# Kernel optimization log

Measured on AMD Instinct MI355X. Metric: run time of the kernel, lower is better.

The kernel has to match this reference:

```python
import jax, jax.numpy as jnp
import numpy as np

B, S, E, H = 2, 2048, 1024, 16
DH = E // H  # 64


def setup_inputs() -> dict:
    key = jax.random.key(0)
    ks = jax.random.split(key, 13)
    s = 1.0 / np.sqrt(E)
    inp = {
        'query': jax.random.normal(ks[0], (B, S, E), jnp.float32),
        'key':   jax.random.normal(ks[1], (B, S, E), jnp.float32),
        'value': jax.random.normal(ks[2], (B, S, E), jnp.float32),
        # nn.Linear weights stored [out, in]
        'Wq': jax.random.uniform(ks[3], (E, E), jnp.float32, -s, s),
        'bq': jax.random.uniform(ks[4], (E,), jnp.float32, -s, s),
        'Wk': jax.random.uniform(ks[5], (E, E), jnp.float32, -s, s),
        'bk': jax.random.uniform(ks[6], (E,), jnp.float32, -s, s),
        'Wv': jax.random.uniform(ks[7], (E, E), jnp.float32, -s, s),
        'bv': jax.random.uniform(ks[8], (E,), jnp.float32, -s, s),
        # 1x1 Conv2d over head channels: weight [H, H] (squeezed from [H,H,1,1]), bias [H]
        'Wc': jax.random.uniform(ks[9], (H, H), jnp.float32, -1.0 / np.sqrt(H), 1.0 / np.sqrt(H)),
        'bc': jax.random.uniform(ks[10], (H,), jnp.float32, -1.0 / np.sqrt(H), 1.0 / np.sqrt(H)),
        'Wo': jax.random.uniform(ks[11], (E, E), jnp.float32, -s, s),
        'bo': jax.random.uniform(ks[12], (E,), jnp.float32, -s, s),
    }
    return inp


def reference(query, key, value, Wq, bq, Wk, bk, Wv, bv, Wc, bc, Wo, bo):
    b, s = query.shape[0], query.shape[1]
    # projections -> (B, H, S, Dh)
    def split_heads(x):
        return x.reshape(b, s, H, DH).transpose(0, 2, 1, 3)
    Q = split_heads(query @ Wq.T + bq)
    K = split_heads(key @ Wk.T + bk)
    V = split_heads(value @ Wv.T + bv)
    # raw scores (B, H, S, S)
    scores = jnp.einsum('bhqd,bhkd->bhqk', Q, K) / np.sqrt(DH).astype(np.float32)
    # 1x1 conv mixes logits across heads: channel-wise matmul + bias
    noise = jnp.einsum('gh,bhqk->bgqk', Wc, scores) + bc[None, :, None, None]
    scores = scores + noise
    weights = jax.nn.softmax(scores, axis=-1)
    out = jnp.einsum('bhqk,bhkd->bhqd', weights, V)  # (B, H, S, Dh)
    out = out.transpose(0, 2, 1, 3).reshape(b, s, E)
    return out @ Wo.T + bo
```

## Files before the change

kernel.cpp:

```cpp
#include <hip/hip_runtime.h>


typedef __attribute__((ext_vector_type(8))) short bf16x8_t;
typedef __attribute__((ext_vector_type(4))) short bf16x4_t;
typedef __attribute__((ext_vector_type(4))) float f32x4_t;

__device__ inline unsigned short f2bf(float f) {
  unsigned u = __builtin_bit_cast(unsigned, f);
  u += 0x7fffu + ((u >> 16) & 1u);
  return (unsigned short)(u >> 16);
}

__device__ inline void bar_lds() {
  asm volatile("s_waitcnt lgkmcnt(0)" ::: "memory");
  __builtin_amdgcn_s_barrier();
}

struct ConvArgs {
  const float* src[7];
  unsigned short* dst[7];
  int n[7];
};

__global__ __launch_bounds__(256) void convert_f32_bf16(ConvArgs a) {
  const int which = blockIdx.y;
  const int i = (blockIdx.x * 256 + threadIdx.x) * 8;
  if (i >= a.n[which]) return;
  const float* s = a.src[which] + i;
  f32x4_t x0 = *(const f32x4_t*)(s);
  f32x4_t x1 = *(const f32x4_t*)(s + 4);
  bf16x8_t o;
#pragma unroll
  for (int j = 0; j < 4; j++) o[j] = (short)f2bf(x0[j]);
#pragma unroll
  for (int j = 0; j < 4; j++) o[4 + j] = (short)f2bf(x1[j]);
  *(bf16x8_t*)(a.dst[which] + i) = o;
}

__global__ __launch_bounds__(256) void gemm_bt(
    const unsigned short* __restrict__ A, const unsigned short* __restrict__ Bt,
    const float* __restrict__ bias, void* __restrict__ C,
    int M, int N, int K, int c_is_f32)
{
  __shared__ unsigned short As[128 * 32];
  __shared__ unsigned short Bs[128 * 32];
  const int t = threadIdx.x;
  const int l = t & 63;
  const int w = t >> 6;
  const int quad = l >> 4, n16 = l & 15;
  const int wm = (w & 1) * 64, wn = (w >> 1) * 64;
  const long m0 = (long)blockIdx.x * 128, n0 = (long)blockIdx.y * 128;

  f32x4_t acc[4][4] = {};

  const unsigned short* gA = A + (m0 + (t >> 2)) * (long)K + (t & 3) * 8;
  const unsigned short* gB = Bt + (n0 + (t >> 2)) * (long)K + (t & 3) * 8;
  const long rowskip = 64l * K;

  bf16x8_t ra0 = *(const bf16x8_t*)(gA);
  bf16x8_t ra1 = *(const bf16x8_t*)(gA + rowskip);
  bf16x8_t rb0 = *(const bf16x8_t*)(gB);
  bf16x8_t rb1 = *(const bf16x8_t*)(gB + rowskip);

  for (int kt = 0; kt < K; kt += 32) {
    bf16x8_t na0, na1, nb0, nb1;
    if (kt + 32 < K) {
      na0 = *(const bf16x8_t*)(gA + kt + 32);
      na1 = *(const bf16x8_t*)(gA + kt + 32 + rowskip);
      nb0 = *(const bf16x8_t*)(gB + kt + 32);
      nb1 = *(const bf16x8_t*)(gB + kt + 32 + rowskip);
    }
    bar_lds();
    *(bf16x8_t*)&As[t * 8] = ra0;
    *(bf16x8_t*)&As[2048 + t * 8] = ra1;
    *(bf16x8_t*)&Bs[t * 8] = rb0;
    *(bf16x8_t*)&Bs[2048 + t * 8] = rb1;
    bar_lds();
    bf16x8_t af[4], bfr[4];
#pragma unroll
    for (int i = 0; i < 4; i++) {
      af[i]  = *(const bf16x8_t*)&As[(wm + i * 16 + n16) * 32 + quad * 8];
      bfr[i] = *(const bf16x8_t*)&Bs[(wn + i * 16 + n16) * 32 + quad * 8];
    }
#pragma unroll
    for (int mi = 0; mi < 4; mi++)
#pragma unroll
      for (int ni = 0; ni < 4; ni++)
        acc[mi][ni] = __builtin_amdgcn_mfma_f32_16x16x32_bf16(af[mi], bfr[ni], acc[mi][ni], 0, 0, 0);
    ra0 = na0; ra1 = na1; rb0 = nb0; rb1 = nb1;
  }

#pragma unroll
  for (int ni = 0; ni < 4; ni++) {
    const long n = n0 + wn + ni * 16 + n16;
    const float bv = bias[n];
#pragma unroll
    for (int mi = 0; mi < 4; mi++) {
#pragma unroll
      for (int r = 0; r < 4; r++) {
        const long m = m0 + wm + mi * 16 + quad * 4 + r;
        const float v = acc[mi][ni][r] + bv;
        if (c_is_f32) ((float*)C)[m * N + n] = v;
        else ((unsigned short*)C)[m * N + n] = f2bf(v);
      }
    }
  }
}

__global__ __launch_bounds__(256) void transpose_v(
    const unsigned short* __restrict__ V, unsigned short* __restrict__ VT)
{
  __shared__ unsigned short tile[64][72];
  const int t = threadIdx.x;
  const int s0 = blockIdx.x * 64, h = blockIdx.y, b = blockIdx.z;
#pragma unroll
  for (int r = 0; r < 2; r++) {
    const int elem = r * 2048 + t * 8;
    const int s = elem >> 6, d = elem & 63;
    *(bf16x8_t*)&tile[s][d] =
        *(const bf16x8_t*)&V[(size_t)(b * 2048 + s0 + s) * 1024 + h * 64 + d];
  }
  __syncthreads();
#pragma unroll
  for (int r = 0; r < 2; r++) {
    const int elem = r * 2048 + t * 8;
    const int d = elem >> 6, sl = elem & 63;
    bf16x8_t o;
#pragma unroll
    for (int j = 0; j < 8; j++) o[j] = (short)tile[sl + j][d];
    *(bf16x8_t*)&VT[((size_t)(b * 16 + h) * 64 + d) * 2048 + s0 + sl] = o;
  }
}

__global__ __launch_bounds__(1024, 4) void attention_fused(
    const unsigned short* __restrict__ Qb, const unsigned short* __restrict__ Kb,
    const unsigned short* __restrict__ VT, const float* __restrict__ Wc,
    unsigned short* __restrict__ Obuf)
{
  __shared__ unsigned short sraw[2][512 * 36];
  __shared__ unsigned short pbuf[2][16 * 580];
  __shared__ float alphabuf[2][16 * 17];
  __shared__ float lbuf[16 * 17];
  __shared__ unsigned short mmat[256];

  const int t = threadIdx.x;
  const int g = t >> 6, l = t & 63;
  const int quad = l >> 4, n16 = l & 15;

  const int id = blockIdx.x;
  const int xcd = id & 7;
  const int b = xcd >> 2;
  const int qb = (xcd & 3) * 32 + (id >> 3);
  const int q0 = qb * 16;

  for (int i = t; i < 2 * 512 * 36; i += 1024) (&sraw[0][0])[i] = 0;
  if (t < 256) {
    const float v = ((((t >> 4) == (t & 15)) ? 1.0f : 0.0f) + Wc[t]) * 0.1803368801111204f;
    mmat[t] = f2bf(v);
  }
  __syncthreads();

  bf16x8_t mfrag;
  if (quad < 2) mfrag = *(const bf16x8_t*)&mmat[n16 * 16 + quad * 8];
  else { bf16x8_t z = {0, 0, 0, 0, 0, 0, 0, 0}; mfrag = z; }
  const int c7 = g >> 2;

  bf16x8_t qf[2];
#pragma unroll
  for (int dr = 0; dr < 2; dr++)
    qf[dr] = *(const bf16x8_t*)&Qb[(size_t)(b * 2048 + q0 + n16) * 1024 + g * 64 + dr * 32 + quad * 8];

  const int slot = g ^ (quad << 3);
  const unsigned short* kptr = Kb + (size_t)(b * 2048 + n16) * 1024 + g * 64 + quad * 8;
  const unsigned short* vptr = VT + ((size_t)(b * 16 + g) * 64 + n16) * 2048 + quad * 8;

  bf16x8_t kf[2][2], vf[4];
  auto load_kf = [&](int kt) {
#pragma unroll
    for (int kc = 0; kc < 2; kc++)
#pragma unroll
      for (int dr = 0; dr < 2; dr++)
        kf[kc][dr] = *(const bf16x8_t*)(kptr + (size_t)(kt + kc * 16) * 1024 + dr * 32);
  };
  auto load_vf = [&](int kt) {
#pragma unroll
    for (int dc = 0; dc < 4; dc++)
      vf[dc] = *(const bf16x8_t*)(vptr + (size_t)dc * 16 * 2048 + kt);
  };
  auto qk_stage = [&](unsigned short* dst) {
    f32x4_t sf[2] = {};
#pragma unroll
    for (int kc = 0; kc < 2; kc++)
#pragma unroll
      for (int dr = 0; dr < 2; dr++)
        sf[kc] = __builtin_amdgcn_mfma_f32_16x16x32_bf16(qf[dr], kf[kc][dr], sf[kc], 0, 0, 0);
#pragma unroll
    for (int kc = 0; kc < 2; kc++)
#pragma unroll
      for (int r = 0; r < 4; r++)
        dst[((quad * 4 + r) * 32 + kc * 16 + n16) * 36 + slot] = f2bf(sf[kc][r]);
  };

  load_kf(0);
  qk_stage(&sraw[0][0]);
  load_kf(32);
  bar_lds();

  f32x4_t o[4] = {};
  float m_run = -1e30f, l_run = 0.0f;

  for (int it = 0; it < 64; ++it) {
    const int cur = it & 1;
    const int oth = cur ^ 1;

    if (it > 0) {
#pragma unroll
      for (int r = 0; r < 4; r++) {
        const float ar = alphabuf[oth][g * 17 + quad * 4 + r];
#pragma unroll
        for (int dc = 0; dc < 4; dc++) o[dc][r] *= ar;
      }
      const unsigned short* pp = &pbuf[oth][g * 580 + n16 * 36 + quad * 8];
      bf16x4_t plo = *(const bf16x4_t*)pp;
      bf16x4_t phi = *(const bf16x4_t*)(pp + 4);
      bf16x8_t pf = {plo[0], plo[1], plo[2], plo[3], phi[0], phi[1], phi[2], phi[3]};
#pragma unroll
      for (int dc = 0; dc < 4; dc++)
        o[dc] = __builtin_amdgcn_mfma_f32_16x16x32_bf16(pf, vf[dc], o[dc], 0, 0, 0);
    }
    load_vf(it * 32);

    f32x4_t mixd[2];
#pragma unroll
    for (int c2 = 0; c2 < 2; c2++) {
      const int c = g * 2 + c2;
      const unsigned short* sp = &sraw[cur][(c * 16 + n16) * 36 + ((quad ^ c7) << 3)];
      bf16x4_t lo = *(const bf16x4_t*)sp;
      bf16x4_t hi = *(const bf16x4_t*)(sp + 4);
      bf16x8_t aa = {lo[0], lo[1], lo[2], lo[3], hi[0], hi[1], hi[2], hi[3]};
      f32x4_t z = {};
      mixd[c2] = __builtin_amdgcn_mfma_f32_16x16x32_bf16(aa, mfrag, z, 0, 0, 0);
    }

    float mx = fmaxf(fmaxf(fmaxf(mixd[0][0], mixd[0][1]), fmaxf(mixd[0][2], mixd[0][3])),
                     fmaxf(fmaxf(mixd[1][0], mixd[1][1]), fmaxf(mixd[1][2], mixd[1][3])));
    mx = fmaxf(mx, __shfl_xor(mx, 16));
    mx = fmaxf(mx, __shfl_xor(mx, 32));
    const float mnew = fmaxf(m_run, mx);
    const float alpha = exp2f(m_run - mnew);
    m_run = mnew;
    float p[2][4];
    float lsum = 0.0f;
#pragma unroll
    for (int c2 = 0; c2 < 2; c2++)
#pragma unroll
      for (int r = 0; r < 4; r++) {
        p[c2][r] = exp2f(mixd[c2][r] - mnew);
        lsum += p[c2][r];
      }
    l_run = l_run * alpha + lsum;

    const int pbase = n16 * 580 + g * 36 + quad * 4;
#pragma unroll
    for (int c2 = 0; c2 < 2; c2++)
#pragma unroll
      for (int rp = 0; rp < 2; rp++) {
        unsigned pk;
        asm volatile("v_cvt_pk_bf16_f32 %0, %1, %2"
                     : "=v"(pk) : "v"(p[c2][2 * rp]), "v"(p[c2][2 * rp + 1]));
        *(unsigned*)&pbuf[cur][pbase + c2 * 16 + 2 * rp] = pk;
      }
    if (quad == 0) alphabuf[cur][n16 * 17 + g] = alpha;

    if (it < 63) qk_stage(&sraw[oth][0]);
    if (it < 62) load_kf((it + 2) * 32);

    bar_lds();
  }

  {
#pragma unroll
    for (int r = 0; r < 4; r++) {
      const float ar = alphabuf[1][g * 17 + quad * 4 + r];
#pragma unroll
      for (int dc = 0; dc < 4; dc++) o[dc][r] *= ar;
    }
    const unsigned short* pp = &pbuf[1][g * 580 + n16 * 36 + quad * 8];
    bf16x4_t plo = *(const bf16x4_t*)pp;
    bf16x4_t phi = *(const bf16x4_t*)(pp + 4);
    bf16x8_t pf = {plo[0], plo[1], plo[2], plo[3], phi[0], phi[1], phi[2], phi[3]};
#pragma unroll
    for (int dc = 0; dc < 4; dc++)
      o[dc] = __builtin_amdgcn_mfma_f32_16x16x32_bf16(pf, vf[dc], o[dc], 0, 0, 0);
  }

  l_run += __shfl_xor(l_run, 16);
  l_run += __shfl_xor(l_run, 32);
  if (quad == 0) lbuf[n16 * 17 + g] = l_run;
  bar_lds();
  float linv[4];
#pragma unroll
  for (int r = 0; r < 4; r++) linv[r] = 1.0f / lbuf[g * 17 + quad * 4 + r];
#pragma unroll
  for (int dc = 0; dc < 4; dc++)
#pragma unroll
    for (int r = 0; r < 4; r++) {
      const float v = o[dc][r] * linv[r];
      Obuf[(size_t)(b * 2048 + q0 + quad * 4 + r) * 1024 + g * 64 + dc * 16 + n16] = f2bf(v);
    }
}

extern "C" void kernel_launch(void* const* d_in, const int* in_sizes, int n_in,
                              void* d_out, int out_size, void* d_ws, size_t ws_size,
                              hipStream_t stream) {
  const float* query = (const float*)d_in[0];
  const float* key   = (const float*)d_in[1];
  const float* value = (const float*)d_in[2];
  const float* Wq = (const float*)d_in[3];
  const float* bq = (const float*)d_in[4];
  const float* Wk = (const float*)d_in[5];
  const float* bk = (const float*)d_in[6];
  const float* Wv = (const float*)d_in[7];
  const float* bv = (const float*)d_in[8];
  const float* Wc = (const float*)d_in[9];
  const float* Wo = (const float*)d_in[11];
  const float* bo = (const float*)d_in[12];

  char* ws = (char*)d_ws;
  const size_t MB = 1024 * 1024;
  unsigned short* q_bf  = (unsigned short*)(ws);
  unsigned short* k_bf  = (unsigned short*)(ws + 8 * MB);
  unsigned short* v_bf  = (unsigned short*)(ws + 16 * MB);
  unsigned short* wq_bf = (unsigned short*)(ws + 24 * MB);
  unsigned short* wk_bf = (unsigned short*)(ws + 26 * MB);
  unsigned short* wv_bf = (unsigned short*)(ws + 28 * MB);
  unsigned short* wo_bf = (unsigned short*)(ws + 30 * MB);
  unsigned short* Qb    = (unsigned short*)(ws + 32 * MB);
  unsigned short* Kb    = (unsigned short*)(ws + 40 * MB);
  unsigned short* Vb    = (unsigned short*)(ws + 48 * MB);
  unsigned short* VT   = k_bf;
  unsigned short* Obuf = q_bf;

  ConvArgs ca;
  ca.src[0] = query; ca.dst[0] = q_bf;  ca.n[0] = 2 * 2048 * 1024;
  ca.src[1] = key;   ca.dst[1] = k_bf;  ca.n[1] = 2 * 2048 * 1024;
  ca.src[2] = value; ca.dst[2] = v_bf;  ca.n[2] = 2 * 2048 * 1024;
  ca.src[3] = Wq;    ca.dst[3] = wq_bf; ca.n[3] = 1024 * 1024;
  ca.src[4] = Wk;    ca.dst[4] = wk_bf; ca.n[4] = 1024 * 1024;
  ca.src[5] = Wv;    ca.dst[5] = wv_bf; ca.n[5] = 1024 * 1024;
  ca.src[6] = Wo;    ca.dst[6] = wo_bf; ca.n[6] = 1024 * 1024;
  convert_f32_bf16<<<dim3(2048, 7), 256, 0, stream>>>(ca);

  gemm_bt<<<dim3(32, 8), 256, 0, stream>>>(q_bf, wq_bf, bq, Qb, 4096, 1024, 1024, 0);
  gemm_bt<<<dim3(32, 8), 256, 0, stream>>>(k_bf, wk_bf, bk, Kb, 4096, 1024, 1024, 0);
  gemm_bt<<<dim3(32, 8), 256, 0, stream>>>(v_bf, wv_bf, bv, Vb, 4096, 1024, 1024, 0);

  transpose_v<<<dim3(32, 16, 2), 256, 0, stream>>>(Vb, VT);

  attention_fused<<<dim3(256), 1024, 0, stream>>>(Qb, Kb, VT, Wc, Obuf);

  gemm_bt<<<dim3(32, 8), 256, 0, stream>>>(Obuf, wo_bf, bo, d_out, 4096, 1024, 1024, 1);
}
```

Measured before the change: 458.6 us.

## Batch QKV GEMMs into one launch and hand-schedule global loads with inline asm

```diff
diff --git a/kernel.cpp b/kernel.cpp
--- a/kernel.cpp
+++ b/kernel.cpp
@@ -10,6 +10,10 @@
   u += 0x7fffu + ((u >> 16) & 1u);
   return (unsigned short)(u >> 16);
 }
+
+#define GLOAD(dst, ptr) \
+  asm volatile("global_load_dwordx4 %0, %1, off" : "=v"(dst) : "v"((const void*)(ptr)))
+#define WAITV0() { asm volatile("s_waitcnt vmcnt(0)"); __builtin_amdgcn_sched_barrier(0); }
 
 __device__ inline void bar_lds() {
   asm volatile("s_waitcnt lgkmcnt(0)" ::: "memory");
@@ -37,13 +41,25 @@
   *(bf16x8_t*)(a.dst[which] + i) = o;
 }
 
-__global__ __launch_bounds__(256) void gemm_bt(
-    const unsigned short* __restrict__ A, const unsigned short* __restrict__ Bt,
-    const float* __restrict__ bias, void* __restrict__ C,
-    int M, int N, int K, int c_is_f32)
+struct GemmArgs {
+  const unsigned short* A[3];
+  const unsigned short* Bt[3];
+  const float* bias[3];
+  void* C[3];
+  int f32out[3];
+};
+
+__global__ __launch_bounds__(256) void gemm_bt(GemmArgs ga, int M, int N, int K)
 {
   __shared__ unsigned short As[128 * 32];
   __shared__ unsigned short Bs[128 * 32];
+  const int z = blockIdx.z;
+  const unsigned short* __restrict__ A  = ga.A[z];
+  const unsigned short* __restrict__ Bt = ga.Bt[z];
+  const float* __restrict__ bias = ga.bias[z];
+  void* __restrict__ C = ga.C[z];
+  const int f32out = ga.f32out[z];
+
   const int t = threadIdx.x;
   const int l = t & 63;
   const int w = t >> 6;
@@ -57,25 +73,22 @@
   const unsigned short* gB = Bt + (n0 + (t >> 2)) * (long)K + (t & 3) * 8;
   const long rowskip = 64l * K;
 
-  bf16x8_t ra0 = *(const bf16x8_t*)(gA);
-  bf16x8_t ra1 = *(const bf16x8_t*)(gA + rowskip);
-  bf16x8_t rb0 = *(const bf16x8_t*)(gB);
-  bf16x8_t rb1 = *(const bf16x8_t*)(gB + rowskip);
+  bf16x8_t ra0, ra1, rb0, rb1;
+  GLOAD(ra0, gA);            GLOAD(ra1, gA + rowskip);
+  GLOAD(rb0, gB);            GLOAD(rb1, gB + rowskip);
+  WAITV0();
 
   for (int kt = 0; kt < K; kt += 32) {
-    bf16x8_t na0, na1, nb0, nb1;
-    if (kt + 32 < K) {
-      na0 = *(const bf16x8_t*)(gA + kt + 32);
-      na1 = *(const bf16x8_t*)(gA + kt + 32 + rowskip);
-      nb0 = *(const bf16x8_t*)(gB + kt + 32);
-      nb1 = *(const bf16x8_t*)(gB + kt + 32 + rowskip);
-    }
     bar_lds();
     *(bf16x8_t*)&As[t * 8] = ra0;
     *(bf16x8_t*)&As[2048 + t * 8] = ra1;
     *(bf16x8_t*)&Bs[t * 8] = rb0;
     *(bf16x8_t*)&Bs[2048 + t * 8] = rb1;
     bar_lds();
+    const long ktn = (kt + 32 < K) ? kt + 32 : 0;
+    GLOAD(ra0, gA + ktn);      GLOAD(ra1, gA + ktn + rowskip);
+    GLOAD(rb0, gB + ktn);      GLOAD(rb1, gB + ktn + rowskip);
+
     bf16x8_t af[4], bfr[4];
 #pragma unroll
     for (int i = 0; i < 4; i++) {
@@ -87,7 +100,7 @@
 #pragma unroll
       for (int ni = 0; ni < 4; ni++)
         acc[mi][ni] = __builtin_amdgcn_mfma_f32_16x16x32_bf16(af[mi], bfr[ni], acc[mi][ni], 0, 0, 0);
-    ra0 = na0; ra1 = na1; rb0 = nb0; rb1 = nb1;
+    WAITV0();
   }
 
 #pragma unroll
@@ -100,7 +113,7 @@
       for (int r = 0; r < 4; r++) {
         const long m = m0 + wm + mi * 16 + quad * 4 + r;
         const float v = acc[mi][ni][r] + bv;
-        if (c_is_f32) ((float*)C)[m * N + n] = v;
+        if (f32out) ((float*)C)[m * N + n] = v;
         else ((unsigned short*)C)[m * N + n] = f2bf(v);
       }
     }
@@ -175,18 +188,6 @@
   const unsigned short* vptr = VT + ((size_t)(b * 16 + g) * 64 + n16) * 2048 + quad * 8;
 
   bf16x8_t kf[2][2], vf[4];
-  auto load_kf = [&](int kt) {
-#pragma unroll
-    for (int kc = 0; kc < 2; kc++)
-#pragma unroll
-      for (int dr = 0; dr < 2; dr++)
-        kf[kc][dr] = *(const bf16x8_t*)(kptr + (size_t)(kt + kc * 16) * 1024 + dr * 32);
-  };
-  auto load_vf = [&](int kt) {
-#pragma unroll
-    for (int dc = 0; dc < 4; dc++)
-      vf[dc] = *(const bf16x8_t*)(vptr + (size_t)dc * 16 * 2048 + kt);
-  };
   auto qk_stage = [&](unsigned short* dst) {
     f32x4_t sf[2] = {};
 #pragma unroll
@@ -201,9 +202,12 @@
         dst[((quad * 4 + r) * 32 + kc * 16 + n16) * 36 + slot] = f2bf(sf[kc][r]);
   };
 
-  load_kf(0);
+#pragma unroll
+  for (int kc = 0; kc < 2; kc++)
+#pragma unroll
+    for (int dr = 0; dr < 2; dr++)
+      kf[kc][dr] = *(const bf16x8_t*)(kptr + (size_t)(kc * 16) * 1024 + dr * 32);
   qk_stage(&sraw[0][0]);
-  load_kf(32);
   bar_lds();
 
   f32x4_t o[4] = {};
@@ -228,7 +232,19 @@
       for (int dc = 0; dc < 4; dc++)
         o[dc] = __builtin_amdgcn_mfma_f32_16x16x32_bf16(pf, vf[dc], o[dc], 0, 0, 0);
     }
-    load_vf(it * 32);
+    __builtin_amdgcn_sched_barrier(0);
+
+    const int kt1 = (it < 63) ? (it + 1) * 32 : 0;
+#pragma unroll
+    for (int kc = 0; kc < 2; kc++)
+#pragma unroll
+      for (int dr = 0; dr < 2; dr++)
+        GLOAD(kf[kc][dr], kptr + (size_t)(kt1 + kc * 16) * 1024 + dr * 32);
+    const int kt = it * 32;
+#pragma unroll
+    for (int dc = 0; dc < 4; dc++)
+      GLOAD(vf[dc], vptr + (size_t)dc * 16 * 2048 + kt);
+    __builtin_amdgcn_sched_barrier(0);
 
     f32x4_t mixd[2];
 #pragma unroll
@@ -266,14 +282,14 @@
 #pragma unroll
       for (int rp = 0; rp < 2; rp++) {
         unsigned pk;
-        asm volatile("v_cvt_pk_bf16_f32 %0, %1, %2"
-                     : "=v"(pk) : "v"(p[c2][2 * rp]), "v"(p[c2][2 * rp + 1]));
+        asm("v_cvt_pk_bf16_f32 %0, %1, %2"
+            : "=v"(pk) : "v"(p[c2][2 * rp]), "v"(p[c2][2 * rp + 1]));
         *(unsigned*)&pbuf[cur][pbase + c2 * 16 + 2 * rp] = pk;
       }
     if (quad == 0) alphabuf[cur][n16 * 17 + g] = alpha;
 
+    WAITV0();
     if (it < 63) qk_stage(&sraw[oth][0]);
-    if (it < 62) load_kf((it + 2) * 32);
 
     bar_lds();
   }
@@ -351,13 +367,19 @@
   ca.src[6] = Wo;    ca.dst[6] = wo_bf; ca.n[6] = 1024 * 1024;
   convert_f32_bf16<<<dim3(2048, 7), 256, 0, stream>>>(ca);
 
-  gemm_bt<<<dim3(32, 8), 256, 0, stream>>>(q_bf, wq_bf, bq, Qb, 4096, 1024, 1024, 0);
-  gemm_bt<<<dim3(32, 8), 256, 0, stream>>>(k_bf, wk_bf, bk, Kb, 4096, 1024, 1024, 0);
-  gemm_bt<<<dim3(32, 8), 256, 0, stream>>>(v_bf, wv_bf, bv, Vb, 4096, 1024, 1024, 0);
+  GemmArgs g3;
+  g3.A[0] = q_bf; g3.Bt[0] = wq_bf; g3.bias[0] = bq; g3.C[0] = Qb; g3.f32out[0] = 0;
+  g3.A[1] = k_bf; g3.Bt[1] = wk_bf; g3.bias[1] = bk; g3.C[1] = Kb; g3.f32out[1] = 0;
+  g3.A[2] = v_bf; g3.Bt[2] = wv_bf; g3.bias[2] = bv; g3.C[2] = Vb; g3.f32out[2] = 0;
+  gemm_bt<<<dim3(32, 8, 3), 256, 0, stream>>>(g3, 4096, 1024, 1024);
 
   transpose_v<<<dim3(32, 16, 2), 256, 0, stream>>>(Vb, VT);
 
   attention_fused<<<dim3(256), 1024, 0, stream>>>(Qb, Kb, VT, Wc, Obuf);
 
-  gemm_bt<<<dim3(32, 8), 256, 0, stream>>>(Obuf, wo_bf, bo, d_out, 4096, 1024, 1024, 1);
-}
+  GemmArgs g1;
+  g1.A[0] = Obuf; g1.Bt[0] = wo_bf; g1.bias[0] = bo; g1.C[0] = d_out; g1.f32out[0] = 1;
+  g1.A[1] = g1.A[0]; g1.Bt[1] = g1.Bt[0]; g1.bias[1] = g1.bias[0]; g1.C[1] = g1.C[0]; g1.f32out[1] = 1;
+  g1.A[2] = g1.A[0]; g1.Bt[2] = g1.Bt[0]; g1.bias[2] = g1.bias[0]; g1.C[2] = g1.C[0]; g1.f32out[2] = 1;
+  gemm_bt<<<dim3(32, 8, 1), 256, 0, stream>>>(g1, 4096, 1024, 1024);
+}
```

After: 462.0 us. Within noise of the previous version (+0.7%).
